# Kernel tuning notes

Hardware: AMD Instinct MI355X
Metric: run time of the kernel (lower is better)

The kernel has to match this reference:

```python
import jax, jax.numpy as jnp
import numpy as np

N = 100000
E = 1600000
IN_C, HID_C, OUT_C = 128, 128, 64


def setup_inputs() -> dict:
    key = jax.random.key(0)
    k_x, k_e, k_w1, k_w2 = jax.random.split(key, 4)
    x = jax.random.normal(k_x, (N, IN_C), dtype=jnp.float32)
    edge_index = jax.random.randint(k_e, (2, E), 0, N, dtype=jnp.int32)
    # nn.Linear default init: U(-1/sqrt(fan_in), 1/sqrt(fan_in)); bias init zeros per module
    lim1 = 1.0 / np.sqrt(IN_C)
    lim2 = 1.0 / np.sqrt(HID_C)
    W1 = jax.random.uniform(k_w1, (IN_C, HID_C), minval=-lim1, maxval=lim1, dtype=jnp.float32)
    b1 = jnp.zeros((HID_C,), dtype=jnp.float32)
    W2 = jax.random.uniform(k_w2, (HID_C, OUT_C), minval=-lim2, maxval=lim2, dtype=jnp.float32)
    b2 = jnp.zeros((OUT_C,), dtype=jnp.float32)
    return {"x": x, "edge_index": edge_index, "W1": W1, "b1": b1, "W2": W2, "b2": b2}


def _out_degree_gcn_conv(x, src, dst, W, b, n_nodes):
    # linear projection (no bias in lin)
    h = x @ W  # [N, out_c]
    # out-degree of each source node
    deg = jax.ops.segment_sum(jnp.ones((src.shape[0],), dtype=h.dtype), src, num_segments=n_nodes)
    deg_inv = 1.0 / jnp.maximum(deg, 1.0)  # clamp(min=1)
    h = h * deg_inv[:, None]
    # message: x_j = h[src]; aggregate: sum at dst
    out = jax.ops.segment_sum(h[src], dst, num_segments=n_nodes)  # [N, out_c]
    return out + b


def reference(x, edge_index, W1, b1, W2, b2):
    src, dst = edge_index[0], edge_index[1]
    n = x.shape[0]
    h = _out_degree_gcn_conv(x, src, dst, W1, b1, n)
    h = jax.nn.relu(h)
    # dropout p=0.0 -> identity
    out = _out_degree_gcn_conv(h, src, dst, W2, b2, n)
    return out
```

## Files before the change

### kernel.cpp

```cpp
#include <hip/hip_runtime.h>
#include <hip/hip_bf16.h>


typedef __attribute__((ext_vector_type(8))) short short8;
typedef __attribute__((ext_vector_type(4))) float floatx4;

__device__ inline unsigned short f2bf(float f) {
    union { float f; unsigned u; } v; v.f = f;
    unsigned r = v.u + 0x7FFF + ((v.u >> 16) & 1);
    return (unsigned short)(r >> 16);
}
__device__ inline float bf2f(unsigned b) {
    union { unsigned u; float f; } v; v.u = b << 16;
    return v.f;
}
__device__ inline float bf2f_hi(unsigned b) {
    union { unsigned u; float f; } v; v.u = b & 0xFFFF0000u;
    return v.f;
}

#define NBMAX 512
#define CAP   8192

__global__ __launch_bounds__(256) void convw_kernel(
    const float* __restrict__ W1, const float* __restrict__ W2,
    unsigned short* __restrict__ Wb1, unsigned short* __restrict__ Wb2,
    int* __restrict__ cnt)
{
    int i = blockIdx.x * 256 + threadIdx.x;
    if (i < NBMAX * 32) cnt[i] = 0;
    if (i < 128 * 128) {
        int k = i >> 7, n = i & 127;
        Wb1[n * 128 + k] = f2bf(W1[k * 128 + n]);
    }
    i -= 128 * 128;
    if (i >= 0 && i < 128 * 64) {
        int k = i >> 6, n = i & 63;
        Wb2[n * 128 + k] = f2bf(W2[k * 64 + n]);
    }
}

__global__ __launch_bounds__(256) void scatter2_kernel(
    const int* __restrict__ src, const int* __restrict__ dst, int E,
    int* __restrict__ cnt_d, int* __restrict__ cnt_s,
    unsigned* __restrict__ pairs, unsigned char* __restrict__ srcs_b, int NB)
{
    __shared__ int hd[NBMAX], bd[NBMAX], cd_[NBMAX];
    __shared__ int hs[NBMAX], bs[NBMAX], cs_[NBMAX];
    for (int i = threadIdx.x; i < NB; i += 256) { hd[i] = 0; cd_[i] = 0; hs[i] = 0; cs_[i] = 0; }
    __syncthreads();
    const int e0 = blockIdx.x * 8192;
    const int e1 = min(e0 + 8192, E);
    for (int i = e0 + threadIdx.x; i < e1; i += 256) {
        atomicAdd(&hd[dst[i] >> 8], 1);
        atomicAdd(&hs[src[i] >> 8], 1);
    }
    __syncthreads();
    for (int i = threadIdx.x; i < NB; i += 256) {
        if (hd[i]) bd[i] = atomicAdd(&cnt_d[i * 16], hd[i]);
        if (hs[i]) bs[i] = atomicAdd(&cnt_s[i * 16], hs[i]);
    }
    __syncthreads();
    for (int i = e0 + threadIdx.x; i < e1; i += 256) {
        int sv = src[i], dv = dst[i];
        int b = dv >> 8;
        int slot = atomicAdd(&cd_[b], 1);
        pairs[(size_t)b * CAP + bd[b] + slot] = ((unsigned)(dv & 255) << 24) | (unsigned)sv;
        int b2 = sv >> 8;
        int slot2 = atomicAdd(&cs_[b2], 1);
        srcs_b[(size_t)b2 * CAP + bs[b2] + slot2] = (unsigned char)(sv & 255);
    }
}

__global__ __launch_bounds__(256) void bucket_finalize_kernel(
    const unsigned* __restrict__ pairs, const unsigned char* __restrict__ srcs_b,
    const int* __restrict__ cnt_d, const int* __restrict__ cnt_s,
    int* __restrict__ sorted_src, int2* __restrict__ se,
    float* __restrict__ deg_inv, int N)
{
    const int b = blockIdx.x;
    const int node0 = b << 8;
    const int t = threadIdx.x;
    const size_t base = (size_t)b * CAP;
    __shared__ int hist[256];
    __shared__ int cur[256];
    __shared__ int pre[256];

    const int cd = cnt_d[b * 16];
    hist[t] = 0;
    __syncthreads();
    for (int i = t; i < cd; i += 256)
        atomicAdd(&hist[pairs[base + i] >> 24], 1);
    __syncthreads();
    int v = hist[t];
    int v4 = (v + 3) & ~3;
    pre[t] = v4;
    __syncthreads();
    for (int o = 1; o < 256; o <<= 1) {
        int add = (t >= o) ? pre[t - o] : 0;
        __syncthreads();
        pre[t] += add;
        __syncthreads();
    }
    int excl = pre[t] - v4;
    cur[t] = excl;
    if (node0 + t < N) {
        se[node0 + t] = make_int2((int)base + excl, (int)base + excl + v);
        for (int i = v; i < v4; ++i) sorted_src[base + excl + i] = N;
    }
    __syncthreads();
    for (int i = t; i < cd; i += 256) {
        unsigned p = pairs[base + i];
        int pos = atomicAdd(&cur[p >> 24], 1);
        sorted_src[base + pos] = (int)(p & 0xFFFFFFu);
    }

    __syncthreads();
    hist[t] = 0;
    __syncthreads();
    const int cs = cnt_s[b * 16];
    for (int i = t; i < cs; i += 256)
        atomicAdd(&hist[srcs_b[base + i]], 1);
    __syncthreads();
    if (node0 + t < N) {
        int d = hist[t];
        deg_inv[node0 + t] = 1.0f / (float)(d < 1 ? 1 : d);
    }
}

template <int NC, int AF>
__global__ __launch_bounds__(256) void gemm_mfma_kernel(
    const void* __restrict__ Ap, const unsigned short* __restrict__ Wb,
    const float* __restrict__ scale, unsigned short* __restrict__ Cb, int M)
{
    constexpr int NT = NC / 16;
    const int t = threadIdx.x;
    if (blockIdx.x == 0 && t < NC / 2)
        ((unsigned*)Cb)[(size_t)M * (NC / 2) + t] = 0;
    const int wm = t >> 6;
    const int lane = t & 63;
    const int lm = lane & 15;
    const int lk = (lane >> 4) * 8;

    const int r0 = blockIdx.x * 64 + wm * 16;
    int row = r0 + lm;
    if (row >= M) row = M - 1;

    floatx4 acc[NT];
#pragma unroll
    for (int j = 0; j < NT; ++j) acc[j] = (floatx4){0.f, 0.f, 0.f, 0.f};

#pragma unroll
    for (int kk = 0; kk < 4; ++kk) {
        const int kb = kk * 32 + lk;
        short8 af;
        if (AF) {
            const float* arow = (const float*)Ap + (size_t)row * 128 + kb;
            float4 a0 = *(const float4*)arow;
            float4 a1 = *(const float4*)(arow + 4);
            af[0] = (short)f2bf(a0.x); af[1] = (short)f2bf(a0.y);
            af[2] = (short)f2bf(a0.z); af[3] = (short)f2bf(a0.w);
            af[4] = (short)f2bf(a1.x); af[5] = (short)f2bf(a1.y);
            af[6] = (short)f2bf(a1.z); af[7] = (short)f2bf(a1.w);
        } else {
            af = *(const short8*)&((const unsigned short*)Ap)[(size_t)row * 128 + kb];
        }
#pragma unroll
        for (int j = 0; j < NT; ++j) {
            short8 bfr = *(const short8*)&Wb[(size_t)(j * 16 + lm) * 128 + kb];
            acc[j] = __builtin_amdgcn_mfma_f32_16x16x32_bf16(af, bfr, acc[j], 0, 0, 0);
        }
    }

    const int rbase = r0 + (lane >> 4) * 4;
#pragma unroll
    for (int reg = 0; reg < 4; ++reg) {
        int rg = rbase + reg;
        if (rg < M) {
            float di = AF ? scale[rg] : 1.0f;
#pragma unroll
            for (int j = 0; j < NT; ++j)
                Cb[(size_t)rg * NC + j * 16 + lm] = f2bf(AF ? acc[j][reg] * di : acc[j][reg]);
        }
    }
}

#define LD128(vv, ii) uint2 vv = *(const uint2*)&val[(size_t)(ii) * 64 + 2 * l]
#define ACC8_128(I0, I1) do { \
    LD128(v0, I0.x); LD128(v1, I0.y); LD128(v2, I0.z); LD128(v3, I0.w); \
    LD128(v4, I1.x); LD128(v5, I1.y); LD128(v6, I1.z); LD128(v7, I1.w); \
    a0 += ((bf2f(v0.x & 0xFFFF) + bf2f(v1.x & 0xFFFF)) + (bf2f(v2.x & 0xFFFF) + bf2f(v3.x & 0xFFFF))) \
        + ((bf2f(v4.x & 0xFFFF) + bf2f(v5.x & 0xFFFF)) + (bf2f(v6.x & 0xFFFF) + bf2f(v7.x & 0xFFFF))); \
    a1 += ((bf2f_hi(v0.x) + bf2f_hi(v1.x)) + (bf2f_hi(v2.x) + bf2f_hi(v3.x))) \
        + ((bf2f_hi(v4.x) + bf2f_hi(v5.x)) + (bf2f_hi(v6.x) + bf2f_hi(v7.x))); \
    a2 += ((bf2f(v0.y & 0xFFFF) + bf2f(v1.y & 0xFFFF)) + (bf2f(v2.y & 0xFFFF) + bf2f(v3.y & 0xFFFF))) \
        + ((bf2f(v4.y & 0xFFFF) + bf2f(v5.y & 0xFFFF)) + (bf2f(v6.y & 0xFFFF) + bf2f(v7.y & 0xFFFF))); \
    a3 += ((bf2f_hi(v0.y) + bf2f_hi(v1.y)) + (bf2f_hi(v2.y) + bf2f_hi(v3.y))) \
        + ((bf2f_hi(v4.y) + bf2f_hi(v5.y)) + (bf2f_hi(v6.y) + bf2f_hi(v7.y))); \
} while (0)
#define ACC4_128(I0) do { \
    LD128(v0, I0.x); LD128(v1, I0.y); LD128(v2, I0.z); LD128(v3, I0.w); \
    a0 += (bf2f(v0.x & 0xFFFF) + bf2f(v1.x & 0xFFFF)) + (bf2f(v2.x & 0xFFFF) + bf2f(v3.x & 0xFFFF)); \
    a1 += (bf2f_hi(v0.x) + bf2f_hi(v1.x)) + (bf2f_hi(v2.x) + bf2f_hi(v3.x)); \
    a2 += (bf2f(v0.y & 0xFFFF) + bf2f(v1.y & 0xFFFF)) + (bf2f(v2.y & 0xFFFF) + bf2f(v3.y & 0xFFFF)); \
    a3 += (bf2f_hi(v0.y) + bf2f_hi(v1.y)) + (bf2f_hi(v2.y) + bf2f_hi(v3.y)); \
} while (0)

__global__ __launch_bounds__(256) void aggregate128_kernel(
    const int2* __restrict__ se, const int* __restrict__ sorted_src,
    const unsigned* __restrict__ val, const float* __restrict__ bias,
    const float* __restrict__ deg_inv, unsigned* __restrict__ outb, int N)
{
    int node = blockIdx.x * 8 + (threadIdx.x >> 5);
    if (node >= N) return;
    int l = threadIdx.x & 31;
    int2 r = se[node];
    int e = r.x;
    const int end4 = r.x + ((r.y - r.x + 3) & ~3);
    float a0 = 0.f, a1 = 0.f, a2 = 0.f, a3 = 0.f;

    if (e + 8 <= end4) {
        int4 i0 = *(const int4*)&sorted_src[e];
        int4 i1 = *(const int4*)&sorted_src[e + 4];
        for (; e + 16 <= end4; e += 8) {
            int4 n0 = *(const int4*)&sorted_src[e + 8];
            int4 n1 = *(const int4*)&sorted_src[e + 12];
            ACC8_128(i0, i1);
            i0 = n0; i1 = n1;
        }
        ACC8_128(i0, i1);
        e += 8;
    }
    if (e < end4) {
        int4 i0 = *(const int4*)&sorted_src[e];
        ACC4_128(i0);
    }

    float di = deg_inv[node];
    float4 bv = *(const float4*)&bias[4 * l];
    a0 = fmaxf(a0 + bv.x, 0.f) * di;
    a1 = fmaxf(a1 + bv.y, 0.f) * di;
    a2 = fmaxf(a2 + bv.z, 0.f) * di;
    a3 = fmaxf(a3 + bv.w, 0.f) * di;
    uint2 o;
    o.x = (unsigned)f2bf(a0) | ((unsigned)f2bf(a1) << 16);
    o.y = (unsigned)f2bf(a2) | ((unsigned)f2bf(a3) << 16);
    *(uint2*)&outb[(size_t)node * 64 + 2 * l] = o;
}

#define LD64(vv, ii) unsigned vv = val[(size_t)(ii) * 32 + l]
#define ACC8_64(I0, I1) do { \
    LD64(v0, I0.x); LD64(v1, I0.y); LD64(v2, I0.z); LD64(v3, I0.w); \
    LD64(v4, I1.x); LD64(v5, I1.y); LD64(v6, I1.z); LD64(v7, I1.w); \
    ax += ((bf2f(v0 & 0xFFFF) + bf2f(v1 & 0xFFFF)) + (bf2f(v2 & 0xFFFF) + bf2f(v3 & 0xFFFF))) \
        + ((bf2f(v4 & 0xFFFF) + bf2f(v5 & 0xFFFF)) + (bf2f(v6 & 0xFFFF) + bf2f(v7 & 0xFFFF))); \
    ay += ((bf2f_hi(v0) + bf2f_hi(v1)) + (bf2f_hi(v2) + bf2f_hi(v3))) \
        + ((bf2f_hi(v4) + bf2f_hi(v5)) + (bf2f_hi(v6) + bf2f_hi(v7))); \
} while (0)
#define ACC4_64(I0) do { \
    LD64(v0, I0.x); LD64(v1, I0.y); LD64(v2, I0.z); LD64(v3, I0.w); \
    ax += (bf2f(v0 & 0xFFFF) + bf2f(v1 & 0xFFFF)) + (bf2f(v2 & 0xFFFF) + bf2f(v3 & 0xFFFF)); \
    ay += (bf2f_hi(v0) + bf2f_hi(v1)) + (bf2f_hi(v2) + bf2f_hi(v3)); \
} while (0)

__global__ __launch_bounds__(256) void aggregate64_kernel(
    const int2* __restrict__ se, const int* __restrict__ sorted_src,
    const unsigned* __restrict__ val, const float* __restrict__ bias,
    float* __restrict__ out, int N)
{
    int node = blockIdx.x * 8 + (threadIdx.x >> 5);
    if (node >= N) return;
    int l = threadIdx.x & 31;
    int2 r = se[node];
    int e = r.x;
    const int end4 = r.x + ((r.y - r.x + 3) & ~3);
    float ax = 0.f, ay = 0.f;

    if (e + 8 <= end4) {
        int4 i0 = *(const int4*)&sorted_src[e];
        int4 i1 = *(const int4*)&sorted_src[e + 4];
        for (; e + 16 <= end4; e += 8) {
            int4 n0 = *(const int4*)&sorted_src[e + 8];
            int4 n1 = *(const int4*)&sorted_src[e + 12];
            ACC8_64(i0, i1);
            i0 = n0; i1 = n1;
        }
        ACC8_64(i0, i1);
        e += 8;
    }
    if (e < end4) {
        int4 i0 = *(const int4*)&sorted_src[e];
        ACC4_64(i0);
    }

    float2 o = make_float2(ax + bias[2 * l], ay + bias[2 * l + 1]);
    *(float2*)&out[(size_t)node * 64 + 2 * l] = o;
}

extern "C" void kernel_launch(void* const* d_in, const int* in_sizes, int n_in,
                              void* d_out, int out_size, void* d_ws, size_t ws_size,
                              hipStream_t stream) {
    const float* x  = (const float*)d_in[0];
    const int*   ei = (const int*)d_in[1];
    const float* W1 = (const float*)d_in[2];
    const float* b1 = (const float*)d_in[3];
    const float* W2 = (const float*)d_in[4];
    const float* b2 = (const float*)d_in[5];
    float* out = (float*)d_out;

    const int N = in_sizes[0] / 128;
    const int E = in_sizes[1] / 2;
    const int* src = ei;
    const int* dst = ei + E;
    const int NB = (N + 255) >> 8;

    char* ws = (char*)d_ws;
    size_t off = 0;
    auto alloc = [&](size_t bytes) {
        void* p = ws + off;
        off = (off + bytes + 255) & ~(size_t)255;
        return p;
    };
    float* deg_inv  = (float*)alloc((size_t)N * 4);
    int2*  se       = (int2*)alloc((size_t)N * 8);
    int*   cnt_d    = (int*)alloc((size_t)NBMAX * 16 * 4 * 2);
    int*   cnt_s    = cnt_d + (size_t)NBMAX * 16;
    unsigned short* Wb1 = (unsigned short*)alloc((size_t)128 * 128 * 2);
    unsigned short* Wb2 = (unsigned short*)alloc((size_t)64 * 128 * 2);
    unsigned*      pairs  = (unsigned*)alloc((size_t)NBMAX * CAP * 4);
    unsigned char* srcs_b = (unsigned char*)alloc((size_t)NBMAX * CAP);
    int*   sorted_src = (int*)alloc((size_t)NBMAX * CAP * 4);
    unsigned short* h    = (unsigned short*)alloc((size_t)(N + 1) * 128 * 2);
    unsigned short* out1 = (unsigned short*)alloc((size_t)N * 128 * 2);
    unsigned short* g = ((size_t)(N + 1) * 128 <= (size_t)NBMAX * CAP * 4)
                            ? (unsigned short*)pairs
                            : (unsigned short*)alloc((size_t)(N + 1) * 64 * 2);

    convw_kernel<<<96, 256, 0, stream>>>(W1, W2, Wb1, Wb2, cnt_d);
    scatter2_kernel<<<(E + 8191) / 8192, 256, 0, stream>>>(src, dst, E, cnt_d, cnt_s,
                                                           pairs, srcs_b, NB);
    bucket_finalize_kernel<<<NB, 256, 0, stream>>>(pairs, srcs_b, cnt_d, cnt_s,
                                                   sorted_src, se, deg_inv, N);

    const int gblocks = (N + 63) / 64;
    gemm_mfma_kernel<128, 1><<<gblocks, 256, 0, stream>>>(x, Wb1, deg_inv, h, N);
    aggregate128_kernel<<<(N + 7) / 8, 256, 0, stream>>>(se, sorted_src, (const unsigned*)h, b1,
                                                         deg_inv, (unsigned*)out1, N);
    gemm_mfma_kernel<64, 0><<<gblocks, 256, 0, stream>>>(out1, Wb2, nullptr, g, N);
    aggregate64_kernel<<<(N + 7) / 8, 256, 0, stream>>>(se, sorted_src, (const unsigned*)g, b2, out, N);
}
```

Baseline: 302.4 us.

## Overlap x-to-bf16 conversion with edge scatter and batch nodes per aggregate block

```diff
diff --git a/kernel.cpp b/kernel.cpp
--- a/kernel.cpp
+++ b/kernel.cpp
@@ -7,8 +7,7 @@
 
 __device__ inline unsigned short f2bf(float f) {
     union { float f; unsigned u; } v; v.f = f;
-    unsigned r = v.u + 0x7FFF + ((v.u >> 16) & 1);
-    return (unsigned short)(r >> 16);
+    return (unsigned short)((v.u + 0x8000u) >> 16);
 }
 __device__ inline float bf2f(unsigned b) {
     union { unsigned u; float f; } v; v.u = b << 16;
@@ -43,8 +42,24 @@
 __global__ __launch_bounds__(256) void scatter2_kernel(
     const int* __restrict__ src, const int* __restrict__ dst, int E,
     int* __restrict__ cnt_d, int* __restrict__ cnt_s,
-    unsigned* __restrict__ pairs, unsigned char* __restrict__ srcs_b, int NB)
-{
+    unsigned* __restrict__ pairs, unsigned char* __restrict__ srcs_b, int NB,
+    const float* __restrict__ x, unsigned short* __restrict__ xb, int NF8)
+{
+    const int EB = (E + 8191) / 8192;
+    if ((int)blockIdx.x >= EB) {
+        int i = ((int)blockIdx.x - EB) * 256 + threadIdx.x;
+        if (i < NF8) {
+            float4 a0 = ((const float4*)x)[(size_t)i * 2];
+            float4 a1 = ((const float4*)x)[(size_t)i * 2 + 1];
+            uint4 st;
+            st.x = (unsigned)f2bf(a0.x) | ((unsigned)f2bf(a0.y) << 16);
+            st.y = (unsigned)f2bf(a0.z) | ((unsigned)f2bf(a0.w) << 16);
+            st.z = (unsigned)f2bf(a1.x) | ((unsigned)f2bf(a1.y) << 16);
+            st.w = (unsigned)f2bf(a1.z) | ((unsigned)f2bf(a1.w) << 16);
+            ((uint4*)xb)[i] = st;
+        }
+        return;
+    }
     __shared__ int hd[NBMAX], bd[NBMAX], cd_[NBMAX];
     __shared__ int hs[NBMAX], bs[NBMAX], cs_[NBMAX];
     for (int i = threadIdx.x; i < NB; i += 256) { hd[i] = 0; cd_[i] = 0; hs[i] = 0; cs_[i] = 0; }
@@ -128,9 +143,9 @@
     }
 }
 
-template <int NC, int AF>
+template <int NC, int SC>
 __global__ __launch_bounds__(256) void gemm_mfma_kernel(
-    const void* __restrict__ Ap, const unsigned short* __restrict__ Wb,
+    const unsigned short* __restrict__ Ab, const unsigned short* __restrict__ Wb,
     const float* __restrict__ scale, unsigned short* __restrict__ Cb, int M)
 {
     constexpr int NT = NC / 16;
@@ -153,18 +168,7 @@
 #pragma unroll
     for (int kk = 0; kk < 4; ++kk) {
         const int kb = kk * 32 + lk;
-        short8 af;
-        if (AF) {
-            const float* arow = (const float*)Ap + (size_t)row * 128 + kb;
-            float4 a0 = *(const float4*)arow;
-            float4 a1 = *(const float4*)(arow + 4);
-            af[0] = (short)f2bf(a0.x); af[1] = (short)f2bf(a0.y);
-            af[2] = (short)f2bf(a0.z); af[3] = (short)f2bf(a0.w);
-            af[4] = (short)f2bf(a1.x); af[5] = (short)f2bf(a1.y);
-            af[6] = (short)f2bf(a1.z); af[7] = (short)f2bf(a1.w);
-        } else {
-            af = *(const short8*)&((const unsigned short*)Ap)[(size_t)row * 128 + kb];
-        }
+        short8 af = *(const short8*)&Ab[(size_t)row * 128 + kb];
 #pragma unroll
         for (int j = 0; j < NT; ++j) {
             short8 bfr = *(const short8*)&Wb[(size_t)(j * 16 + lm) * 128 + kb];
@@ -177,10 +181,10 @@
     for (int reg = 0; reg < 4; ++reg) {
         int rg = rbase + reg;
         if (rg < M) {
-            float di = AF ? scale[rg] : 1.0f;
+            float di = SC ? scale[rg] : 1.0f;
 #pragma unroll
             for (int j = 0; j < NT; ++j)
-                Cb[(size_t)rg * NC + j * 16 + lm] = f2bf(AF ? acc[j][reg] * di : acc[j][reg]);
+                Cb[(size_t)rg * NC + j * 16 + lm] = f2bf(SC ? acc[j][reg] * di : acc[j][reg]);
         }
     }
 }
@@ -211,41 +215,44 @@
     const unsigned* __restrict__ val, const float* __restrict__ bias,
     const float* __restrict__ deg_inv, unsigned* __restrict__ outb, int N)
 {
-    int node = blockIdx.x * 8 + (threadIdx.x >> 5);
-    if (node >= N) return;
-    int l = threadIdx.x & 31;
-    int2 r = se[node];
-    int e = r.x;
-    const int end4 = r.x + ((r.y - r.x + 3) & ~3);
-    float a0 = 0.f, a1 = 0.f, a2 = 0.f, a3 = 0.f;
-
-    if (e + 8 <= end4) {
-        int4 i0 = *(const int4*)&sorted_src[e];
-        int4 i1 = *(const int4*)&sorted_src[e + 4];
-        for (; e + 16 <= end4; e += 8) {
-            int4 n0 = *(const int4*)&sorted_src[e + 8];
-            int4 n1 = *(const int4*)&sorted_src[e + 12];
+    const int hw = threadIdx.x >> 5;
+    const int l = threadIdx.x & 31;
+    for (int g = 0; g < 4; ++g) {
+        int node = blockIdx.x * 32 + g * 8 + hw;
+        if (node >= N) continue;
+        int2 r = se[node];
+        int e = r.x;
+        const int end4 = r.x + ((r.y - r.x + 3) & ~3);
+        float a0 = 0.f, a1 = 0.f, a2 = 0.f, a3 = 0.f;
+
+        if (e + 8 <= end4) {
+            int4 i0 = *(const int4*)&sorted_src[e];
+            int4 i1 = *(const int4*)&sorted_src[e + 4];
+            for (; e + 16 <= end4; e += 8) {
+                int4 n0 = *(const int4*)&sorted_src[e + 8];
+                int4 n1 = *(const int4*)&sorted_src[e + 12];
+                ACC8_128(i0, i1);
+                i0 = n0; i1 = n1;
+            }
             ACC8_128(i0, i1);
-            i0 = n0; i1 = n1;
-        }
-        ACC8_128(i0, i1);
-        e += 8;
-    }
-    if (e < end4) {
-        int4 i0 = *(const int4*)&sorted_src[e];
-        ACC4_128(i0);
-    }
-
-    float di = deg_inv[node];
-    float4 bv = *(const float4*)&bias[4 * l];
-    a0 = fmaxf(a0 + bv.x, 0.f) * di;
-    a1 = fmaxf(a1 + bv.y, 0.f) * di;
-    a2 = fmaxf(a2 + bv.z, 0.f) * di;
-    a3 = fmaxf(a3 + bv.w, 0.f) * di;
-    uint2 o;
-    o.x = (unsigned)f2bf(a0) | ((unsigned)f2bf(a1) << 16);
-    o.y = (unsigned)f2bf(a2) | ((unsigned)f2bf(a3) << 16);
-    *(uint2*)&outb[(size_t)node * 64 + 2 * l] = o;
+            e += 8;
+        }
+        if (e < end4) {
+            int4 i0 = *(const int4*)&sorted_src[e];
+            ACC4_128(i0);
+        }
+
+        float di = deg_inv[node];
+        float4 bv = *(const float4*)&bias[4 * l];
+        a0 = fmaxf(a0 + bv.x, 0.f) * di;
+        a1 = fmaxf(a1 + bv.y, 0.f) * di;
+        a2 = fmaxf(a2 + bv.z, 0.f) * di;
+        a3 = fmaxf(a3 + bv.w, 0.f) * di;
+        uint2 o;
+        o.x = (unsigned)f2bf(a0) | ((unsigned)f2bf(a1) << 16);
+        o.y = (unsigned)f2bf(a2) | ((unsigned)f2bf(a3) << 16);
+        *(uint2*)&outb[(size_t)node * 64 + 2 * l] = o;
+    }
 }
 
 #define LD64(vv, ii) unsigned vv = val[(size_t)(ii) * 32 + l]
@@ -268,33 +275,36 @@
     const unsigned* __restrict__ val, const float* __restrict__ bias,
     float* __restrict__ out, int N)
 {
-    int node = blockIdx.x * 8 + (threadIdx.x >> 5);
-    if (node >= N) return;
-    int l = threadIdx.x & 31;
-    int2 r = se[node];
-    int e = r.x;
-    const int end4 = r.x + ((r.y - r.x + 3) & ~3);
-    float ax = 0.f, ay = 0.f;
-
-    if (e + 8 <= end4) {
-        int4 i0 = *(const int4*)&sorted_src[e];
-        int4 i1 = *(const int4*)&sorted_src[e + 4];
-        for (; e + 16 <= end4; e += 8) {
-            int4 n0 = *(const int4*)&sorted_src[e + 8];
-            int4 n1 = *(const int4*)&sorted_src[e + 12];
+    const int hw = threadIdx.x >> 5;
+    const int l = threadIdx.x & 31;
+    for (int g = 0; g < 4; ++g) {
+        int node = blockIdx.x * 32 + g * 8 + hw;
+        if (node >= N) continue;
+        int2 r = se[node];
+        int e = r.x;
+        const int end4 = r.x + ((r.y - r.x + 3) & ~3);
+        float ax = 0.f, ay = 0.f;
+
+        if (e + 8 <= end4) {
+            int4 i0 = *(const int4*)&sorted_src[e];
+            int4 i1 = *(const int4*)&sorted_src[e + 4];
+            for (; e + 16 <= end4; e += 8) {
+                int4 n0 = *(const int4*)&sorted_src[e + 8];
+                int4 n1 = *(const int4*)&sorted_src[e + 12];
+                ACC8_64(i0, i1);
+                i0 = n0; i1 = n1;
+            }
             ACC8_64(i0, i1);
-            i0 = n0; i1 = n1;
-        }
-        ACC8_64(i0, i1);
-        e += 8;
-    }
-    if (e < end4) {
-        int4 i0 = *(const int4*)&sorted_src[e];
-        ACC4_64(i0);
-    }
-
-    float2 o = make_float2(ax + bias[2 * l], ay + bias[2 * l + 1]);
-    *(float2*)&out[(size_t)node * 64 + 2 * l] = o;
+            e += 8;
+        }
+        if (e < end4) {
+            int4 i0 = *(const int4*)&sorted_src[e];
+            ACC4_64(i0);
+        }
+
+        float2 o = make_float2(ax + bias[2 * l], ay + bias[2 * l + 1]);
+        *(float2*)&out[(size_t)node * 64 + 2 * l] = o;
+    }
 }
 
 extern "C" void kernel_launch(void* const* d_in, const int* in_sizes, int n_in,
@@ -332,20 +342,26 @@
     int*   sorted_src = (int*)alloc((size_t)NBMAX * CAP * 4);
     unsigned short* h    = (unsigned short*)alloc((size_t)(N + 1) * 128 * 2);
     unsigned short* out1 = (unsigned short*)alloc((size_t)N * 128 * 2);
+    unsigned short* xb = out1;
     unsigned short* g = ((size_t)(N + 1) * 128 <= (size_t)NBMAX * CAP * 4)
                             ? (unsigned short*)pairs
                             : (unsigned short*)alloc((size_t)(N + 1) * 64 * 2);
 
     convw_kernel<<<96, 256, 0, stream>>>(W1, W2, Wb1, Wb2, cnt_d);
-    scatter2_kernel<<<(E + 8191) / 8192, 256, 0, stream>>>(src, dst, E, cnt_d, cnt_s,
-                                                           pairs, srcs_b, NB);
+
+    const int EB = (E + 8191) / 8192;
+    const int NF8 = (N * 128) / 8;
+    const int CB = (NF8 + 255) / 256;
+    scatter2_kernel<<<EB + CB, 256, 0, stream>>>(src, dst, E, cnt_d, cnt_s,
+                                                 pairs, srcs_b, NB, x, xb, NF8);
     bucket_finalize_kernel<<<NB, 256, 0, stream>>>(pairs, srcs_b, cnt_d, cnt_s,
                                                    sorted_src, se, deg_inv, N);
 
     const int gblocks = (N + 63) / 64;
-    gemm_mfma_kernel<128, 1><<<gblocks, 256, 0, stream>>>(x, Wb1, deg_inv, h, N);
-    aggregate128_kernel<<<(N + 7) / 8, 256, 0, stream>>>(se, sorted_src, (const unsigned*)h, b1,
-                                                         deg_inv, (unsigned*)out1, N);
+    const int ablocks = (N + 31) / 32;
+    gemm_mfma_kernel<128, 1><<<gblocks, 256, 0, stream>>>(xb, Wb1, deg_inv, h, N);
+    aggregate128_kernel<<<ablocks, 256, 0, stream>>>(se, sorted_src, (const unsigned*)h, b1,
+                                                     deg_inv, (unsigned*)out1, N);
     gemm_mfma_kernel<64, 0><<<gblocks, 256, 0, stream>>>(out1, Wb2, nullptr, g, N);
-    aggregate64_kernel<<<(N + 7) / 8, 256, 0, stream>>>(se, sorted_src, (const unsigned*)g, b2, out, N);
-}
+    aggregate64_kernel<<<ablocks, 256, 0, stream>>>(se, sorted_src, (const unsigned*)g, b2, out, N);
+}
```

New measurement: 316.8 us. 1.05x slower.
